# Performance work log

Measured on AMD Instinct MI355X. Metric: run time of the kernel, lower is better.

Reference implementation:

```python
import jax, jax.numpy as jnp
import numpy as np

BINS = 10
LOSS_WEIGHT = 1.0


def setup_inputs() -> dict:
    key = jax.random.key(0)
    k1, k2, k3 = jax.random.split(key, 3)
    N, C = 262144, 80
    pred = jax.random.normal(k1, (N, C), dtype=jnp.float32)
    # binary class targets (sparse positives, as in detection)
    target = (jax.random.uniform(k2, (N, C)) < 0.02).astype(jnp.float32)
    # 1 = valid sample, 0 = ignored
    label_weight = (jax.random.uniform(k3, (N, C)) < 0.95).astype(jnp.float32)
    return {"pred": pred, "target": target, "label_weight": label_weight}


def reference(pred, target, label_weight):
    # GHM-C loss, momentum=0 path (no EMA buffer).
    valid = label_weight > 0
    validf = valid.astype(jnp.float32)
    tot = jnp.maximum(jnp.sum(validf), 1.0)

    # gradient norm g = |sigmoid(pred).detach() - target|, in [0, 1]
    g = jnp.abs(jax.lax.stop_gradient(jax.nn.sigmoid(pred)) - target)
    # edges are i/BINS with last edge 1+1e-6, so bin i covers [i/B, (i+1)/B);
    # equivalent to floor(g*B) clipped to [0, B-1] (g==1 lands in last bin).
    bin_idx = jnp.clip(jnp.floor(g * BINS).astype(jnp.int32), 0, BINS - 1)

    # per-bin counts over valid elements (single-pass histogram)
    counts = jax.ops.segment_sum(validf.reshape(-1), bin_idx.reshape(-1),
                                 num_segments=BINS)
    n = jnp.sum(counts > 0).astype(jnp.float32)  # number of non-empty bins
    per_bin_w = jnp.where(counts > 0, tot / jnp.maximum(counts, 1.0), 0.0)
    weights = per_bin_w[bin_idx] * validf  # scattered weight assignment
    weights = jnp.where(n > 0, weights / n, weights)

    # binary_cross_entropy_with_logits, elementwise: softplus(x) - x*t
    bce = jax.nn.softplus(pred) - pred * target
    loss = jnp.sum(bce * weights) / tot
    return loss * LOSS_WEIGHT
```

## Files before the change

kernel.cpp:

```cpp
#include <hip/hip_runtime.h>

#define BINS 10


__global__ __launch_bounds__(64) void ghmc_zero(float* ws_sum, int* ws_cnt) {
    int i = threadIdx.x;
    if (i < BINS) { ws_sum[i] = 0.0f; ws_cnt[i] = 0; }
}

__device__ __forceinline__ void ghmc_elem(float pk, float tk, float wk,
                                          float lsum[BINS], int lcnt[BINS]) {
    if (wk > 0.0f) {
        float e = __expf(-fabsf(pk));
        float r = 1.0f / (1.0f + e);
        float s = (pk >= 0.0f) ? r : (1.0f - r);
        float g = fabsf(s - tk);
        int bin = (int)(g * 10.0f);
        bin = bin > (BINS - 1) ? (BINS - 1) : bin;
        float bce = fmaxf(pk, 0.0f) + log1pf(e) - pk * tk;
#pragma unroll
        for (int b = 0; b < BINS; ++b) {
            if (bin == b) { lsum[b] += bce; lcnt[b] += 1; }
        }
    }
}

__global__ __launch_bounds__(256) void ghmc_main(
    const float* __restrict__ pred, const float* __restrict__ targ,
    const float* __restrict__ lw,
    float* __restrict__ ws_sum, int* __restrict__ ws_cnt, int n) {

    float lsum[BINS];
    int   lcnt[BINS];
#pragma unroll
    for (int b = 0; b < BINS; ++b) { lsum[b] = 0.0f; lcnt[b] = 0; }

    const int tid    = blockIdx.x * blockDim.x + threadIdx.x;
    const int stride = gridDim.x * blockDim.x;
    const int nvec   = n >> 2;

    const float4* p4 = (const float4*)pred;
    const float4* t4 = (const float4*)targ;
    const float4* w4 = (const float4*)lw;

    for (int i = tid; i < nvec; i += stride) {
        float4 p = p4[i], t = t4[i], w = w4[i];
        const float* pp = (const float*)&p;
        const float* tt = (const float*)&t;
        const float* ww = (const float*)&w;
#pragma unroll
        for (int k = 0; k < 4; ++k)
            ghmc_elem(pp[k], tt[k], ww[k], lsum, lcnt);
    }
    {
        int rem = n & 3;
        if (tid < rem) {
            int i = (nvec << 2) + tid;
            ghmc_elem(pred[i], targ[i], lw[i], lsum, lcnt);
        }
    }

    __shared__ float s_sum[BINS];
    __shared__ int   s_cnt[BINS];
    if (threadIdx.x < BINS) { s_sum[threadIdx.x] = 0.0f; s_cnt[threadIdx.x] = 0; }
    __syncthreads();

    const int lane = threadIdx.x & 63;
#pragma unroll
    for (int b = 0; b < BINS; ++b) {
        float s = lsum[b];
        int   c = lcnt[b];
#pragma unroll
        for (int off = 32; off > 0; off >>= 1) {
            s += __shfl_xor(s, off, 64);
            c += __shfl_xor(c, off, 64);
        }
        if (lane == 0) {
            atomicAdd(&s_sum[b], s);
            atomicAdd(&s_cnt[b], c);
        }
    }
    __syncthreads();

    if (threadIdx.x < BINS) {
        float s = s_sum[threadIdx.x];
        int   c = s_cnt[threadIdx.x];
        if (c != 0) {
            atomicAdd(&ws_sum[threadIdx.x], s);
            atomicAdd(&ws_cnt[threadIdx.x], c);
        }
    }
}

__global__ __launch_bounds__(64) void ghmc_finalize(
    const float* __restrict__ ws_sum, const int* __restrict__ ws_cnt,
    float* __restrict__ out) {
    if (threadIdx.x == 0) {
        float acc = 0.0f;
        int n = 0;
        for (int b = 0; b < BINS; ++b) {
            int c = ws_cnt[b];
            if (c > 0) { n += 1; acc += ws_sum[b] / (float)c; }
        }
        out[0] = (n > 0) ? (acc / (float)n) : 0.0f;
    }
}

extern "C" void kernel_launch(void* const* d_in, const int* in_sizes, int n_in,
                              void* d_out, int out_size, void* d_ws, size_t ws_size,
                              hipStream_t stream) {
    const float* pred = (const float*)d_in[0];
    const float* targ = (const float*)d_in[1];
    const float* lw   = (const float*)d_in[2];
    float* out = (float*)d_out;
    const int n = in_sizes[0];

    float* ws_sum = (float*)d_ws;
    int*   ws_cnt = (int*)((char*)d_ws + BINS * sizeof(float));

    ghmc_zero<<<1, 64, 0, stream>>>(ws_sum, ws_cnt);

    const int threads = 256;
    const int blocks  = 2048;
    ghmc_main<<<blocks, threads, 0, stream>>>(pred, targ, lw, ws_sum, ws_cnt, n);

    ghmc_finalize<<<1, 64, 0, stream>>>(ws_sum, ws_cnt, out);
}
```

Baseline: 282.4 us.

## Bin by logit thresholds with cumulative wave-ballot counts and per-block partials

Replaces the sigmoid-based bin index with comparisons of the sign-adjusted logit against precomputed logit thresholds, accumulating cumulative (>= threshold) sums and wave-wide ballot/popcount counts, then differencing adjacent cumulative bins in the finalize step. BCE is rewritten as softplus of the sign-flipped logit using fast exp/log. Global atomics and the zero kernel are replaced by per-block partial rows that a single-block finalize kernel reduces. The aim is to drop the divide, log1p and per-bin branch chain and the launch and atomic overhead. Counts are carried as floats, and the cumulative differencing can lose precision, which may shift results slightly near bin edges.

```diff
diff --git a/kernel.cpp b/kernel.cpp
--- a/kernel.cpp
+++ b/kernel.cpp
@@ -3,40 +3,22 @@
 #define BINS 10
 
 
-__global__ __launch_bounds__(64) void ghmc_zero(float* ws_sum, int* ws_cnt) {
-    int i = threadIdx.x;
-    if (i < BINS) { ws_sum[i] = 0.0f; ws_cnt[i] = 0; }
-}
-
-__device__ __forceinline__ void ghmc_elem(float pk, float tk, float wk,
-                                          float lsum[BINS], int lcnt[BINS]) {
-    if (wk > 0.0f) {
-        float e = __expf(-fabsf(pk));
-        float r = 1.0f / (1.0f + e);
-        float s = (pk >= 0.0f) ? r : (1.0f - r);
-        float g = fabsf(s - tk);
-        int bin = (int)(g * 10.0f);
-        bin = bin > (BINS - 1) ? (BINS - 1) : bin;
-        float bce = fmaxf(pk, 0.0f) + log1pf(e) - pk * tk;
-#pragma unroll
-        for (int b = 0; b < BINS; ++b) {
-            if (bin == b) { lsum[b] += bce; lcnt[b] += 1; }
-        }
-    }
-}
-
 __global__ __launch_bounds__(256) void ghmc_main(
     const float* __restrict__ pred, const float* __restrict__ targ,
-    const float* __restrict__ lw,
-    float* __restrict__ ws_sum, int* __restrict__ ws_cnt, int n) {
+    const float* __restrict__ lw, float* __restrict__ part, int n, int grid) {
 
-    float lsum[BINS];
-    int   lcnt[BINS];
+    const float T0 = -2.19722458f, T1 = -1.38629436f, T2 = -0.84729786f,
+                T3 = -0.40546511f, T4 = 0.0f,         T5 =  0.40546511f,
+                T6 =  0.84729786f, T7 =  1.38629436f, T8 =  2.19722458f;
+    const float T[9] = {T0,T1,T2,T3,T4,T5,T6,T7,T8};
+
+    float S[10];
+    int   C[10];
 #pragma unroll
-    for (int b = 0; b < BINS; ++b) { lsum[b] = 0.0f; lcnt[b] = 0; }
+    for (int k = 0; k < 10; ++k) { S[k] = 0.0f; C[k] = 0; }
 
     const int tid    = blockIdx.x * blockDim.x + threadIdx.x;
-    const int stride = gridDim.x * blockDim.x;
+    const int stride = grid * blockDim.x;
     const int nvec   = n >> 2;
 
     const float4* p4 = (const float4*)pred;
@@ -49,60 +31,98 @@
         const float* tt = (const float*)&t;
         const float* ww = (const float*)&w;
 #pragma unroll
-        for (int k = 0; k < 4; ++k)
-            ghmc_elem(pp[k], tt[k], ww[k], lsum, lcnt);
+        for (int e = 0; e < 4; ++e) {
+            float pk = pp[e], tk = tt[e], wk = ww[e];
+            float m  = fmaf(-2.0f, tk, 1.0f);
+            float q  = m * pk;
+            bool  valid = wk > 0.0f;
+            float qm = valid ? q : -1.0e30f;
+            float u  = __expf(-fabsf(q));
+            float bce = fmaxf(q, 0.0f) + __logf(1.0f + u);
+            float bw  = bce * wk;
+            S[0] += bw;
+            C[0] += (int)__popcll(__ballot(valid));
+#pragma unroll
+            for (int j = 0; j < 9; ++j) {
+                bool pr = qm >= T[j];
+                C[j + 1] += (int)__popcll(__ballot(pr));
+                S[j + 1] += pr ? bw : 0.0f;
+            }
+        }
     }
     {
         int rem = n & 3;
         if (tid < rem) {
-            int i = (nvec << 2) + tid;
-            ghmc_elem(pred[i], targ[i], lw[i], lsum, lcnt);
+            int idx = (nvec << 2) + tid;
+            float pk = pred[idx], tk = targ[idx], wk = lw[idx];
+            float m  = fmaf(-2.0f, tk, 1.0f);
+            float q  = m * pk;
+            bool  valid = wk > 0.0f;
+            float qm = valid ? q : -1.0e30f;
+            float u  = __expf(-fabsf(q));
+            float bce = fmaxf(q, 0.0f) + __logf(1.0f + u);
+            float bw  = bce * wk;
+            S[0] += bw;
+            C[0] += (int)__popcll(__ballot(valid));
+#pragma unroll
+            for (int j = 0; j < 9; ++j) {
+                bool pr = qm >= T[j];
+                C[j + 1] += (int)__popcll(__ballot(pr));
+                S[j + 1] += pr ? bw : 0.0f;
+            }
         }
     }
 
-    __shared__ float s_sum[BINS];
-    __shared__ int   s_cnt[BINS];
-    if (threadIdx.x < BINS) { s_sum[threadIdx.x] = 0.0f; s_cnt[threadIdx.x] = 0; }
+    __shared__ float sS[BINS];
+    __shared__ float sC[BINS];
+    if (threadIdx.x < BINS) { sS[threadIdx.x] = 0.0f; sC[threadIdx.x] = 0.0f; }
     __syncthreads();
 
     const int lane = threadIdx.x & 63;
 #pragma unroll
-    for (int b = 0; b < BINS; ++b) {
-        float s = lsum[b];
-        int   c = lcnt[b];
+    for (int k = 0; k < BINS; ++k) {
+        float s = S[k];
 #pragma unroll
-        for (int off = 32; off > 0; off >>= 1) {
-            s += __shfl_xor(s, off, 64);
-            c += __shfl_xor(c, off, 64);
-        }
+        for (int off = 32; off > 0; off >>= 1) s += __shfl_xor(s, off, 64);
         if (lane == 0) {
-            atomicAdd(&s_sum[b], s);
-            atomicAdd(&s_cnt[b], c);
+            atomicAdd(&sS[k], s);
+            atomicAdd(&sC[k], (float)C[k]);
         }
     }
     __syncthreads();
 
     if (threadIdx.x < BINS) {
-        float s = s_sum[threadIdx.x];
-        int   c = s_cnt[threadIdx.x];
-        if (c != 0) {
-            atomicAdd(&ws_sum[threadIdx.x], s);
-            atomicAdd(&ws_cnt[threadIdx.x], c);
-        }
+        part[threadIdx.x * grid + blockIdx.x]          = sS[threadIdx.x];
+        part[(BINS + threadIdx.x) * grid + blockIdx.x] = sC[threadIdx.x];
     }
 }
 
-__global__ __launch_bounds__(64) void ghmc_finalize(
-    const float* __restrict__ ws_sum, const int* __restrict__ ws_cnt,
-    float* __restrict__ out) {
+__global__ __launch_bounds__(256) void ghmc_fin(
+    const float* __restrict__ part, float* __restrict__ out, int grid) {
+    __shared__ float rows[2 * BINS];
+    __shared__ float wsum[4];
+    for (int k = 0; k < 2 * BINS; ++k) {
+        float v = 0.0f;
+        for (int i = threadIdx.x; i < grid; i += 256) v += part[k * grid + i];
+#pragma unroll
+        for (int off = 32; off > 0; off >>= 1) v += __shfl_xor(v, off, 64);
+        if ((threadIdx.x & 63) == 0) wsum[threadIdx.x >> 6] = v;
+        __syncthreads();
+        if (threadIdx.x == 0) rows[k] = wsum[0] + wsum[1] + wsum[2] + wsum[3];
+        __syncthreads();
+    }
     if (threadIdx.x == 0) {
         float acc = 0.0f;
-        int n = 0;
+        int   nb  = 0;
+#pragma unroll
         for (int b = 0; b < BINS; ++b) {
-            int c = ws_cnt[b];
-            if (c > 0) { n += 1; acc += ws_sum[b] / (float)c; }
+            float sN = (b < BINS - 1) ? rows[b + 1]        : 0.0f;
+            float cN = (b < BINS - 1) ? rows[BINS + b + 1] : 0.0f;
+            float s  = rows[b] - sN;
+            float c  = rows[BINS + b] - cN;
+            if (c > 0.5f) { nb += 1; acc += s / c; }
         }
-        out[0] = (n > 0) ? (acc / (float)n) : 0.0f;
+        out[0] = (nb > 0) ? (acc / (float)nb) : 0.0f;
     }
 }
 
@@ -112,17 +132,17 @@
     const float* pred = (const float*)d_in[0];
     const float* targ = (const float*)d_in[1];
     const float* lw   = (const float*)d_in[2];
-    float* out = (float*)d_out;
+    float* out  = (float*)d_out;
+    float* part = (float*)d_ws;
     const int n = in_sizes[0];
 
-    float* ws_sum = (float*)d_ws;
-    int*   ws_cnt = (int*)((char*)d_ws + BINS * sizeof(float));
+    int grid = 2048;
+    size_t need = (size_t)grid * 2 * BINS * sizeof(float);
+    if (ws_size < need) {
+        grid = (int)(ws_size / (2 * BINS * sizeof(float)));
+        if (grid < 1) grid = 1;
+    }
 
-    ghmc_zero<<<1, 64, 0, stream>>>(ws_sum, ws_cnt);
-
-    const int threads = 256;
-    const int blocks  = 2048;
-    ghmc_main<<<blocks, threads, 0, stream>>>(pred, targ, lw, ws_sum, ws_cnt, n);
-
-    ghmc_finalize<<<1, 64, 0, stream>>>(ws_sum, ws_cnt, out);
+    ghmc_main<<<grid, 256, 0, stream>>>(pred, targ, lw, part, n, grid);
+    ghmc_fin<<<1, 256, 0, stream>>>(part, out, grid);
 }
```

After: 294.9 us. 4.4% more time.
